# Optimization experiments

Measured on AMD Instinct MI355X. Metric: run time of the kernel, lower is better.

Reference implementation:

```python
import jax, jax.numpy as jnp
import numpy as np

HEAD_SIZE = 128
N_EMBD = 128
B, T = 16, 2048


def setup_inputs() -> dict:
    key = jax.random.key(0)
    ks = jax.random.split(key, 7)
    s = 1.0 / np.sqrt(N_EMBD)
    return {
        "x": jax.random.normal(ks[0], (B, T, N_EMBD), dtype=jnp.float32),
        "Wq": jax.random.normal(ks[1], (N_EMBD, HEAD_SIZE), dtype=jnp.float32) * s,
        "bq": jax.random.normal(ks[2], (HEAD_SIZE,), dtype=jnp.float32) * s,
        "Wk": jax.random.normal(ks[3], (N_EMBD, HEAD_SIZE), dtype=jnp.float32) * s,
        "bk": jax.random.normal(ks[4], (HEAD_SIZE,), dtype=jnp.float32) * s,
        "Wv": jax.random.normal(ks[5], (N_EMBD, HEAD_SIZE), dtype=jnp.float32) * s,
        "bv": jax.random.normal(ks[6], (HEAD_SIZE,), dtype=jnp.float32) * s,
    }


def reference(x, Wq, bq, Wk, bk, Wv, bv):
    # Q/K/V projections: [B,T,E] @ [E,H] -> [B,T,H]
    q = jnp.einsum("bte,eh->bth", x, Wq) + bq
    k = jnp.einsum("bte,eh->bth", x, Wk) + bk
    v = jnp.einsum("bte,eh->bth", x, Wv) + bv
    scale = 1.0 / (HEAD_SIZE ** 0.5)
    scores = jnp.einsum("bqh,bkh->bqk", q, k) * scale  # [B,T,T]
    t = x.shape[1]
    tril = jnp.tril(jnp.ones((t, t), dtype=scores.dtype))
    # Faithful to original: scores*tril - 1e12*(1-tril)
    scores = scores * tril - 1e12 * (1.0 - tril)
    attn = jax.nn.softmax(scores, axis=-1)
    out = jnp.einsum("bqk,bkh->bqh", attn, v)  # [B,T,H]
    return out
```

## Files before the change

kernel.cpp:

```cpp
#include <hip/hip_runtime.h>
#include <math.h>

#define Bn 16
#define Tn 2048
#define En 128
#define Hn 128

typedef _Float16 f16;
typedef _Float16 f16x8 __attribute__((ext_vector_type(8)));
typedef _Float16 f16x4 __attribute__((ext_vector_type(4)));
typedef float    f32x4 __attribute__((ext_vector_type(4)));

#define MFMA16(a, b, c) __builtin_amdgcn_mfma_f32_16x16x32_f16(a, b, c, 0, 0, 0)

__global__ __launch_bounds__(256) void prep_wt(
    const float* __restrict__ Wq, const float* __restrict__ Wk,
    const float* __restrict__ Wv, f16* __restrict__ Wt)
{
    int id = blockIdx.x * 256 + threadIdx.x;
    int p = id >> 14;
    int rem = id & 16383;
    int nn = rem >> 7, kk = rem & 127;
    const float* W = (p == 0) ? Wq : (p == 1) ? Wk : Wv;
    Wt[id] = (f16)W[kk * Hn + nn];
}

__global__ __launch_bounds__(256) void qkv_proj(
    const float* __restrict__ x, const f16* __restrict__ Wt,
    const float* __restrict__ bq, const float* __restrict__ bk,
    const float* __restrict__ bv,
    f16* __restrict__ Qo, f16* __restrict__ Ko, f16* __restrict__ Vtp)
{
    __shared__ f16 xs[64][En + 8];
    __shared__ f16 wt[Hn][En + 8];

    const int t = threadIdx.x;
    const long row0 = (long)blockIdx.x * 64;

    {
        const float4* xg = (const float4*)(x + row0 * En);
        #pragma unroll
        for (int i = 0; i < 8; ++i) {
            int idx = t + i * 256;
            int r = idx >> 5, c4 = idx & 31;
            float4 v = xg[idx];
            f16x4 h = { (f16)v.x, (f16)v.y, (f16)v.z, (f16)v.w };
            *(f16x4*)&xs[r][c4 * 4] = h;
        }
    }
    __syncthreads();

    const int w = t >> 6, lane = t & 63;
    const int ln = lane & 15, hi = lane >> 4;

    f16x8 xf[4];
    #pragma unroll
    for (int kss = 0; kss < 4; ++kss)
        xf[kss] = *(const f16x8*)&xs[w * 16 + ln][kss * 32 + hi * 8];

    const float* bias[3] = { bq, bk, bv };
    const int b  = (int)(row0 >> 11);
    const int t0 = (int)(row0 & 2047);

    #pragma unroll
    for (int p = 0; p < 3; ++p) {
        __syncthreads();
        {
            const f16x8* wg = (const f16x8*)(Wt + p * En * Hn);
            #pragma unroll
            for (int i = 0; i < 8; ++i) {
                int idx = t + i * 256;
                *(f16x8*)&wt[idx >> 4][(idx & 15) * 8] = wg[idx];
            }
        }
        __syncthreads();

        f32x4 acc[8];
        #pragma unroll
        for (int i = 0; i < 8; ++i) acc[i] = (f32x4){0.f, 0.f, 0.f, 0.f};

        #pragma unroll
        for (int kss = 0; kss < 4; ++kss) {
            #pragma unroll
            for (int nt = 0; nt < 8; ++nt) {
                f16x8 bf = *(const f16x8*)&wt[nt * 16 + ln][kss * 32 + hi * 8];
                acc[nt] = MFMA16(xf[kss], bf, acc[nt]);
            }
        }

        if (p < 2) {
            const float scl = (p == 0) ? 0.08838834764831845f : 1.0f;
            f16* dst = (p == 0) ? Qo : Ko;
            #pragma unroll
            for (int nt = 0; nt < 8; ++nt) {
                int col = nt * 16 + ln;
                float bvv = bias[p][col];
                #pragma unroll
                for (int reg = 0; reg < 4; ++reg) {
                    int rr = w * 16 + hi * 4 + reg;
                    dst[(row0 + rr) * Hn + col] = (f16)((acc[nt][reg] + bvv) * scl);
                }
            }
        } else {
            f16 (*vbuf)[72] = reinterpret_cast<f16(*)[72]>(&wt[0][0]);
            __syncthreads();
            #pragma unroll
            for (int nt = 0; nt < 8; ++nt) {
                int col = nt * 16 + ln;
                float bvv = bias[2][col];
                f16x4 hv;
                #pragma unroll
                for (int reg = 0; reg < 4; ++reg)
                    hv[reg] = (f16)(acc[nt][reg] + bvv);
                *(f16x4*)&vbuf[col][w * 16 + hi * 4] = hv;
            }
            __syncthreads();
            #pragma unroll
            for (int i = 0; i < 4; ++i) {
                int idx = t + i * 256;
                int h = idx >> 3, c = idx & 7;
                *(f16x8*)(Vtp + ((long)b * Hn + h) * Tn + t0 + c * 8) =
                    *(const f16x8*)&vbuf[h][c * 8];
            }
        }
    }
}

__global__ __launch_bounds__(256, 2) void attn_fwd(
    const f16* __restrict__ Qf, const f16* __restrict__ Kf,
    const f16* __restrict__ Vt, float* __restrict__ Out)
{
    __shared__ f16 ksh[2][64][En + 8];
    __shared__ f16 vsh[2][Hn][64 + 8];
    __shared__ f16 psh[4][16][64 + 8];

    const int t = threadIdx.x;
    const int w = t >> 6, lane = t & 63;
    const int ln = lane & 15, hi = lane >> 4;

    const int n = blockIdx.x;
    const int s = n >> 8, r = n & 255;
    const int j = r >> 4, bb = r & 15;
    const int qi = s ? (31 - j) : j;
    const int q0 = qi * 64;
    const int nkt = qi + 1;
    const long qbase = ((long)bb * Tn + q0) * Hn;
    const long kbase = (long)bb * Tn * Hn;
    const long vbase = (long)bb * Hn * Tn;

    f16x8 qfr[4];
    #pragma unroll
    for (int kss = 0; kss < 4; ++kss)
        qfr[kss] = *(const f16x8*)(Qf + qbase + (long)(16 * w + ln) * Hn
                                   + kss * 32 + hi * 8);

    f32x4 oacc[8];
    #pragma unroll
    for (int i = 0; i < 8; ++i) oacc[i] = (f32x4){0.f, 0.f, 0.f, 0.f};
    float mrow[4], lrow[4];
    #pragma unroll
    for (int i = 0; i < 4; ++i) { mrow[i] = -INFINITY; lrow[i] = 0.f; }

    f16x8 kreg[4], vreg[4];
    {
        const f16* Kg = Kf + kbase;
        const f16* Vg = Vt + vbase;
        #pragma unroll
        for (int i = 0; i < 4; ++i) {
            int idx = t + i * 256;
            kreg[i] = *(const f16x8*)(Kg + (long)(idx >> 4) * Hn + (idx & 15) * 8);
            vreg[i] = *(const f16x8*)(Vg + (long)(idx >> 3) * Tn + (idx & 7) * 8);
        }
        #pragma unroll
        for (int i = 0; i < 4; ++i) {
            int idx = t + i * 256;
            *(f16x8*)&ksh[0][idx >> 4][(idx & 15) * 8] = kreg[i];
            *(f16x8*)&vsh[0][idx >> 3][(idx & 7) * 8] = vreg[i];
        }
    }
    __syncthreads();

    int cur = 0;
    for (int kt = 0; kt < nkt; ++kt) {
        const int k0 = kt * 64;
        const bool pre = (kt + 1 < nkt);

        if (pre) {
            const f16* Kg = Kf + kbase + (long)(k0 + 64) * Hn;
            const f16* Vg = Vt + vbase + (k0 + 64);
            #pragma unroll
            for (int i = 0; i < 4; ++i) {
                int idx = t + i * 256;
                kreg[i] = *(const f16x8*)(Kg + (long)(idx >> 4) * Hn + (idx & 15) * 8);
                vreg[i] = *(const f16x8*)(Vg + (long)(idx >> 3) * Tn + (idx & 7) * 8);
            }
        }

        f32x4 sacc[4];
        #pragma unroll
        for (int i = 0; i < 4; ++i) sacc[i] = (f32x4){0.f, 0.f, 0.f, 0.f};
        __builtin_amdgcn_s_setprio(1);
        #pragma unroll
        for (int kss = 0; kss < 4; ++kss) {
            #pragma unroll
            for (int nt = 0; nt < 4; ++nt) {
                f16x8 bf = *(const f16x8*)&ksh[cur][nt * 16 + ln][kss * 32 + hi * 8];
                sacc[nt] = MFMA16(qfr[kss], bf, sacc[nt]);
            }
        }
        __builtin_amdgcn_s_setprio(0);

        const bool diag = (kt == nkt - 1);
        #pragma unroll
        for (int reg = 0; reg < 4; ++reg) {
            int gq = q0 + 16 * w + hi * 4 + reg;
            float s0 = sacc[0][reg], s1 = sacc[1][reg],
                  s2 = sacc[2][reg], s3 = sacc[3][reg];
            if (diag) {
                s0 = (k0 + ln      <= gq) ? s0 : -1e12f;
                s1 = (k0 + ln + 16 <= gq) ? s1 : -1e12f;
                s2 = (k0 + ln + 32 <= gq) ? s2 : -1e12f;
                s3 = (k0 + ln + 48 <= gq) ? s3 : -1e12f;
            }
            float mx = fmaxf(fmaxf(s0, s1), fmaxf(s2, s3));
            mx = fmaxf(mx, __shfl_xor(mx, 1));
            mx = fmaxf(mx, __shfl_xor(mx, 2));
            mx = fmaxf(mx, __shfl_xor(mx, 4));
            mx = fmaxf(mx, __shfl_xor(mx, 8));
            float mnew = fmaxf(mrow[reg], mx);
            float p0 = __expf(s0 - mnew), p1 = __expf(s1 - mnew);
            float p2 = __expf(s2 - mnew), p3 = __expf(s3 - mnew);
            float sm = p0 + p1 + p2 + p3;
            sm += __shfl_xor(sm, 1);
            sm += __shfl_xor(sm, 2);
            sm += __shfl_xor(sm, 4);
            sm += __shfl_xor(sm, 8);
            float f = __expf(mrow[reg] - mnew);
            mrow[reg] = mnew;
            lrow[reg] = lrow[reg] * f + sm;
            #pragma unroll
            for (int nt2 = 0; nt2 < 8; ++nt2) oacc[nt2][reg] *= f;
            int qr = hi * 4 + reg;
            psh[w][qr][ln]      = (f16)p0;
            psh[w][qr][ln + 16] = (f16)p1;
            psh[w][qr][ln + 32] = (f16)p2;
            psh[w][qr][ln + 48] = (f16)p3;
        }

        __builtin_amdgcn_s_setprio(1);
        #pragma unroll
        for (int kss = 0; kss < 2; ++kss) {
            f16x8 pa = *(const f16x8*)&psh[w][ln][kss * 32 + hi * 8];
            #pragma unroll
            for (int nt = 0; nt < 8; ++nt) {
                f16x8 vb = *(const f16x8*)&vsh[cur][nt * 16 + ln][kss * 32 + hi * 8];
                oacc[nt] = MFMA16(pa, vb, oacc[nt]);
            }
        }
        __builtin_amdgcn_s_setprio(0);

        if (pre) {
            #pragma unroll
            for (int i = 0; i < 4; ++i) {
                int idx = t + i * 256;
                *(f16x8*)&ksh[cur ^ 1][idx >> 4][(idx & 15) * 8] = kreg[i];
                *(f16x8*)&vsh[cur ^ 1][idx >> 3][(idx & 7) * 8] = vreg[i];
            }
            __syncthreads();
            cur ^= 1;
        }
    }

    #pragma unroll
    for (int reg = 0; reg < 4; ++reg) {
        float inv = 1.0f / lrow[reg];
        long orow = qbase + (long)(16 * w + hi * 4 + reg) * Hn;
        #pragma unroll
        for (int nt = 0; nt < 8; ++nt)
            Out[orow + nt * 16 + ln] = oacc[nt][reg] * inv;
    }
}

extern "C" void kernel_launch(void* const* d_in, const int* in_sizes, int n_in,
                              void* d_out, int out_size, void* d_ws, size_t ws_size,
                              hipStream_t stream)
{
    const float* x  = (const float*)d_in[0];
    const float* Wq = (const float*)d_in[1];
    const float* bq = (const float*)d_in[2];
    const float* Wk = (const float*)d_in[3];
    const float* bk = (const float*)d_in[4];
    const float* Wv = (const float*)d_in[5];
    const float* bv = (const float*)d_in[6];

    const size_t NE = (size_t)Bn * Tn * Hn;
    f16* Qf = (f16*)d_ws;
    f16* Kf = Qf + NE;
    f16* Vt = Kf + NE;
    f16* Wt = Vt + NE;

    prep_wt<<<dim3(192), dim3(256), 0, stream>>>(Wq, Wk, Wv, Wt);
    qkv_proj<<<dim3((Bn * Tn) / 64), dim3(256), 0, stream>>>(
        x, Wt, bq, bk, bv, Qf, Kf, Vt);
    attn_fwd<<<dim3(512), dim3(256), 0, stream>>>(Qf, Kf, Vt, (float*)d_out);
}
```

Measured before the change: 151.4 us.

## Lazy softmax rescaling with exp2, single-buffered LDS, and coalesced QKV stores

After: 145.3 us. -4.1%, faster.

```diff
diff --git a/kernel.cpp b/kernel.cpp
--- a/kernel.cpp
+++ b/kernel.cpp
@@ -17,15 +17,30 @@
     const float* __restrict__ Wq, const float* __restrict__ Wk,
     const float* __restrict__ Wv, f16* __restrict__ Wt)
 {
-    int id = blockIdx.x * 256 + threadIdx.x;
-    int p = id >> 14;
-    int rem = id & 16383;
-    int nn = rem >> 7, kk = rem & 127;
+    __shared__ f16 lds[En][Hn + 8];
+    const int t = threadIdx.x;
+    const int p = blockIdx.x;
     const float* W = (p == 0) ? Wq : (p == 1) ? Wk : Wv;
-    Wt[id] = (f16)W[kk * Hn + nn];
+
+    #pragma unroll
+    for (int i = 0; i < 16; ++i) {
+        int idx = t + i * 256;
+        int k = idx >> 5, n4 = idx & 31;
+        float4 v = ((const float4*)W)[idx];
+        #pragma unroll
+        for (int j = 0; j < 4; ++j)
+            lds[n4 * 4 + j][k] = (f16)(&v.x)[j];
+    }
+    __syncthreads();
+    #pragma unroll
+    for (int i = 0; i < 8; ++i) {
+        int idx = t + i * 256;
+        int n = idx >> 4, c = idx & 15;
+        *(f16x8*)(Wt + p * En * Hn + n * Hn + c * 8) = *(const f16x8*)&lds[n][c * 8];
+    }
 }
 
-__global__ __launch_bounds__(256) void qkv_proj(
+__global__ __launch_bounds__(256, 2) void qkv_proj(
     const float* __restrict__ x, const f16* __restrict__ Wt,
     const float* __restrict__ bq, const float* __restrict__ bk,
     const float* __restrict__ bv,
@@ -48,6 +63,14 @@
             *(f16x4*)&xs[r][c4 * 4] = h;
         }
     }
+    {
+        const f16x8* wg = (const f16x8*)Wt;
+        #pragma unroll
+        for (int i = 0; i < 8; ++i) {
+            int idx = t + i * 256;
+            *(f16x8*)&wt[idx >> 4][(idx & 15) * 8] = wg[idx];
+        }
+    }
     __syncthreads();
 
     const int w = t >> 6, lane = t & 63;
@@ -64,17 +87,6 @@
 
     #pragma unroll
     for (int p = 0; p < 3; ++p) {
-        __syncthreads();
-        {
-            const f16x8* wg = (const f16x8*)(Wt + p * En * Hn);
-            #pragma unroll
-            for (int i = 0; i < 8; ++i) {
-                int idx = t + i * 256;
-                *(f16x8*)&wt[idx >> 4][(idx & 15) * 8] = wg[idx];
-            }
-        }
-        __syncthreads();
-
         f32x4 acc[8];
         #pragma unroll
         for (int i = 0; i < 8; ++i) acc[i] = (f32x4){0.f, 0.f, 0.f, 0.f};
@@ -87,23 +99,36 @@
                 acc[nt] = MFMA16(xf[kss], bf, acc[nt]);
             }
         }
+        __syncthreads();
 
         if (p < 2) {
-            const float scl = (p == 0) ? 0.08838834764831845f : 1.0f;
-            f16* dst = (p == 0) ? Qo : Ko;
+            const f16x8* wg = (const f16x8*)(Wt + (p + 1) * En * Hn);
+            #pragma unroll
+            for (int i = 0; i < 8; ++i) {
+                int idx = t + i * 256;
+                *(f16x8*)&wt[idx >> 4][(idx & 15) * 8] = wg[idx];
+            }
+            const float scl = (p == 0)
+                ? 0.08838834764831845f * 1.4426950408889634f : 1.0f;
             #pragma unroll
             for (int nt = 0; nt < 8; ++nt) {
                 int col = nt * 16 + ln;
                 float bvv = bias[p][col];
                 #pragma unroll
-                for (int reg = 0; reg < 4; ++reg) {
-                    int rr = w * 16 + hi * 4 + reg;
-                    dst[(row0 + rr) * Hn + col] = (f16)((acc[nt][reg] + bvv) * scl);
-                }
+                for (int reg = 0; reg < 4; ++reg)
+                    xs[w * 16 + hi * 4 + reg][col] =
+                        (f16)((acc[nt][reg] + bvv) * scl);
+            }
+            __syncthreads();
+            f16* dst = (p == 0) ? Qo : Ko;
+            #pragma unroll
+            for (int i = 0; i < 4; ++i) {
+                int idx = t + i * 256;
+                int r = idx >> 4, c = idx & 15;
+                *(f16x8*)(dst + (row0 + r) * Hn + c * 8) = *(const f16x8*)&xs[r][c * 8];
             }
         } else {
             f16 (*vbuf)[72] = reinterpret_cast<f16(*)[72]>(&wt[0][0]);
-            __syncthreads();
             #pragma unroll
             for (int nt = 0; nt < 8; ++nt) {
                 int col = nt * 16 + ln;
@@ -130,8 +155,8 @@
     const f16* __restrict__ Qf, const f16* __restrict__ Kf,
     const f16* __restrict__ Vt, float* __restrict__ Out)
 {
-    __shared__ f16 ksh[2][64][En + 8];
-    __shared__ f16 vsh[2][Hn][64 + 8];
+    __shared__ f16 ksh[64][En + 8];
+    __shared__ f16 vsh[Hn][64 + 8];
     __shared__ f16 psh[4][16][64 + 8];
 
     const int t = threadIdx.x;
@@ -157,34 +182,29 @@
     f32x4 oacc[8];
     #pragma unroll
     for (int i = 0; i < 8; ++i) oacc[i] = (f32x4){0.f, 0.f, 0.f, 0.f};
-    float mrow[4], lrow[4];
-    #pragma unroll
-    for (int i = 0; i < 4; ++i) { mrow[i] = -INFINITY; lrow[i] = 0.f; }
-
-    f16x8 kreg[4], vreg[4];
+    float mrow[4], lpart[4];
+    #pragma unroll
+    for (int i = 0; i < 4; ++i) { mrow[i] = -INFINITY; lpart[i] = 0.f; }
+
     {
         const f16* Kg = Kf + kbase;
         const f16* Vg = Vt + vbase;
         #pragma unroll
         for (int i = 0; i < 4; ++i) {
             int idx = t + i * 256;
-            kreg[i] = *(const f16x8*)(Kg + (long)(idx >> 4) * Hn + (idx & 15) * 8);
-            vreg[i] = *(const f16x8*)(Vg + (long)(idx >> 3) * Tn + (idx & 7) * 8);
-        }
-        #pragma unroll
-        for (int i = 0; i < 4; ++i) {
-            int idx = t + i * 256;
-            *(f16x8*)&ksh[0][idx >> 4][(idx & 15) * 8] = kreg[i];
-            *(f16x8*)&vsh[0][idx >> 3][(idx & 7) * 8] = vreg[i];
+            *(f16x8*)&ksh[idx >> 4][(idx & 15) * 8] =
+                *(const f16x8*)(Kg + (long)(idx >> 4) * Hn + (idx & 15) * 8);
+            *(f16x8*)&vsh[idx >> 3][(idx & 7) * 8] =
+                *(const f16x8*)(Vg + (long)(idx >> 3) * Tn + (idx & 7) * 8);
         }
     }
     __syncthreads();
 
-    int cur = 0;
     for (int kt = 0; kt < nkt; ++kt) {
         const int k0 = kt * 64;
         const bool pre = (kt + 1 < nkt);
 
+        f16x8 kreg[4], vreg[4];
         if (pre) {
             const f16* Kg = Kf + kbase + (long)(k0 + 64) * Hn;
             const f16* Vg = Vt + vbase + (k0 + 64);
@@ -204,42 +224,57 @@
         for (int kss = 0; kss < 4; ++kss) {
             #pragma unroll
             for (int nt = 0; nt < 4; ++nt) {
-                f16x8 bf = *(const f16x8*)&ksh[cur][nt * 16 + ln][kss * 32 + hi * 8];
+                f16x8 bf = *(const f16x8*)&ksh[nt * 16 + ln][kss * 32 + hi * 8];
                 sacc[nt] = MFMA16(qfr[kss], bf, sacc[nt]);
             }
         }
         __builtin_amdgcn_s_setprio(0);
 
         const bool diag = (kt == nkt - 1);
+        float sv[4][4];
         #pragma unroll
         for (int reg = 0; reg < 4; ++reg) {
             int gq = q0 + 16 * w + hi * 4 + reg;
-            float s0 = sacc[0][reg], s1 = sacc[1][reg],
-                  s2 = sacc[2][reg], s3 = sacc[3][reg];
-            if (diag) {
-                s0 = (k0 + ln      <= gq) ? s0 : -1e12f;
-                s1 = (k0 + ln + 16 <= gq) ? s1 : -1e12f;
-                s2 = (k0 + ln + 32 <= gq) ? s2 : -1e12f;
-                s3 = (k0 + ln + 48 <= gq) ? s3 : -1e12f;
-            }
-            float mx = fmaxf(fmaxf(s0, s1), fmaxf(s2, s3));
-            mx = fmaxf(mx, __shfl_xor(mx, 1));
-            mx = fmaxf(mx, __shfl_xor(mx, 2));
-            mx = fmaxf(mx, __shfl_xor(mx, 4));
-            mx = fmaxf(mx, __shfl_xor(mx, 8));
-            float mnew = fmaxf(mrow[reg], mx);
-            float p0 = __expf(s0 - mnew), p1 = __expf(s1 - mnew);
-            float p2 = __expf(s2 - mnew), p3 = __expf(s3 - mnew);
-            float sm = p0 + p1 + p2 + p3;
-            sm += __shfl_xor(sm, 1);
-            sm += __shfl_xor(sm, 2);
-            sm += __shfl_xor(sm, 4);
-            sm += __shfl_xor(sm, 8);
-            float f = __expf(mrow[reg] - mnew);
-            mrow[reg] = mnew;
-            lrow[reg] = lrow[reg] * f + sm;
-            #pragma unroll
-            for (int nt2 = 0; nt2 < 8; ++nt2) oacc[nt2][reg] *= f;
+            #pragma unroll
+            for (int nt = 0; nt < 4; ++nt) {
+                float v = sacc[nt][reg];
+                if (diag) v = (k0 + nt * 16 + ln <= gq) ? v : -1e12f;
+                sv[reg][nt] = v;
+            }
+        }
+
+        float worst = -INFINITY;
+        #pragma unroll
+        for (int reg = 0; reg < 4; ++reg) {
+            float pm = fmaxf(fmaxf(sv[reg][0], sv[reg][1]),
+                             fmaxf(sv[reg][2], sv[reg][3]));
+            worst = fmaxf(worst, pm - mrow[reg]);
+        }
+        if (__any(worst > 11.5415603f)) {
+            #pragma unroll
+            for (int reg = 0; reg < 4; ++reg) {
+                float mx = fmaxf(fmaxf(sv[reg][0], sv[reg][1]),
+                                 fmaxf(sv[reg][2], sv[reg][3]));
+                mx = fmaxf(mx, __shfl_xor(mx, 1));
+                mx = fmaxf(mx, __shfl_xor(mx, 2));
+                mx = fmaxf(mx, __shfl_xor(mx, 4));
+                mx = fmaxf(mx, __shfl_xor(mx, 8));
+                float mnew = fmaxf(mrow[reg], mx);
+                float f = exp2f(mrow[reg] - mnew);
+                mrow[reg] = mnew;
+                lpart[reg] *= f;
+                #pragma unroll
+                for (int nt2 = 0; nt2 < 8; ++nt2) oacc[nt2][reg] *= f;
+            }
+        }
+
+        #pragma unroll
+        for (int reg = 0; reg < 4; ++reg) {
+            float p0 = exp2f(sv[reg][0] - mrow[reg]);
+            float p1 = exp2f(sv[reg][1] - mrow[reg]);
+            float p2 = exp2f(sv[reg][2] - mrow[reg]);
+            float p3 = exp2f(sv[reg][3] - mrow[reg]);
+            lpart[reg] += (p0 + p1) + (p2 + p3);
             int qr = hi * 4 + reg;
             psh[w][qr][ln]      = (f16)p0;
             psh[w][qr][ln + 16] = (f16)p1;
@@ -253,27 +288,32 @@
             f16x8 pa = *(const f16x8*)&psh[w][ln][kss * 32 + hi * 8];
             #pragma unroll
             for (int nt = 0; nt < 8; ++nt) {
-                f16x8 vb = *(const f16x8*)&vsh[cur][nt * 16 + ln][kss * 32 + hi * 8];
+                f16x8 vb = *(const f16x8*)&vsh[nt * 16 + ln][kss * 32 + hi * 8];
                 oacc[nt] = MFMA16(pa, vb, oacc[nt]);
             }
         }
         __builtin_amdgcn_s_setprio(0);
 
+        __syncthreads();
         if (pre) {
             #pragma unroll
             for (int i = 0; i < 4; ++i) {
                 int idx = t + i * 256;
-                *(f16x8*)&ksh[cur ^ 1][idx >> 4][(idx & 15) * 8] = kreg[i];
-                *(f16x8*)&vsh[cur ^ 1][idx >> 3][(idx & 7) * 8] = vreg[i];
+                *(f16x8*)&ksh[idx >> 4][(idx & 15) * 8] = kreg[i];
+                *(f16x8*)&vsh[idx >> 3][(idx & 7) * 8] = vreg[i];
             }
             __syncthreads();
-            cur ^= 1;
         }
     }
 
     #pragma unroll
     for (int reg = 0; reg < 4; ++reg) {
-        float inv = 1.0f / lrow[reg];
+        float lr = lpart[reg];
+        lr += __shfl_xor(lr, 1);
+        lr += __shfl_xor(lr, 2);
+        lr += __shfl_xor(lr, 4);
+        lr += __shfl_xor(lr, 8);
+        float inv = 1.0f / lr;
         long orow = qbase + (long)(16 * w + hi * 4 + reg) * Hn;
         #pragma unroll
         for (int nt = 0; nt < 8; ++nt)
@@ -299,7 +339,7 @@
     f16* Vt = Kf + NE;
     f16* Wt = Vt + NE;
 
-    prep_wt<<<dim3(192), dim3(256), 0, stream>>>(Wq, Wk, Wv, Wt);
+    prep_wt<<<dim3(3), dim3(256), 0, stream>>>(Wq, Wk, Wv, Wt);
     qkv_proj<<<dim3((Bn * Tn) / 64), dim3(256), 0, stream>>>(
         x, Wt, bq, bk, bv, Qf, Kf, Vt);
     attn_fwd<<<dim3(512), dim3(256), 0, stream>>>(Qf, Kf, Vt, (float*)d_out);
```
